# Kernel tuning notes

Measured on AMD Instinct MI355X. Metric: run time of the kernel, lower is better.

Reference implementation:

```python
import jax, jax.numpy as jnp
import numpy as np

N, D = 1024, 1024          # sensors, raw signal length
EMB, CC, TP, NH, L, FF = 128, 64, 16, 4, 2, 2048
HD = EMB // NH             # head dim = 32


def setup_inputs() -> dict:
    key = jax.random.key(0)
    ks = iter(jax.random.split(key, 64))
    rn = lambda shape, s=0.05: jax.random.normal(next(ks), shape, dtype=jnp.float32) * s
    return {
        "x": jax.random.normal(next(ks), (N, 1, D), dtype=jnp.float32),
        "conv1_w": rn((CC // 2, 1, 7), 0.3), "conv1_b": rn((CC // 2,)),
        "bn1_g": jnp.ones((CC // 2,)), "bn1_b": jnp.zeros((CC // 2,)),
        "bn1_m": jnp.zeros((CC // 2,)), "bn1_v": jnp.ones((CC // 2,)),
        "conv2_w": rn((CC, CC // 2, 5), 0.1), "conv2_b": rn((CC,)),
        "bn2_g": jnp.ones((CC,)), "bn2_b": jnp.zeros((CC,)),
        "bn2_m": jnp.zeros((CC,)), "bn2_v": jnp.ones((CC,)),
        "proj_w": rn((EMB, CC * TP)), "proj_b": rn((EMB,)),
        "attn_in_w": rn((L, 3 * EMB, EMB)), "attn_in_b": rn((L, 3 * EMB)),
        "attn_out_w": rn((L, EMB, EMB)), "attn_out_b": rn((L, EMB)),
        "ln1_g": jnp.ones((L, EMB)), "ln1_b": jnp.zeros((L, EMB)),
        "ff1_w": rn((L, FF, EMB)), "ff1_b": rn((L, FF)),
        "ff2_w": rn((L, EMB, FF)), "ff2_b": rn((L, EMB)),
        "ln2_g": jnp.ones((L, EMB)), "ln2_b": jnp.zeros((L, EMB)),
        "nh1_w": rn((EMB, EMB)), "nh1_b": rn((EMB,)),
        "nh2_w": rn((3, EMB)), "nh2_b": rn((3,)),
        "e1_w": rn((EMB, 2 * EMB)), "e1_b": rn((EMB,)),
        "e2_w": rn((1, EMB)), "e2_b": rn((1,)),
        "p1_w": rn((EMB, EMB)), "p1_b": rn((EMB,)),
        "p2_w": rn((EMB, EMB)), "p2_b": rn((EMB,)),
    }


def _conv1d(x, w, b, pad):
    y = jax.lax.conv_general_dilated(x, w, (1,), [(pad, pad)],
                                     dimension_numbers=("NCH", "OIH", "NCH"))
    return y + b[None, :, None]


def _bn(x, g, b, m, v):  # eval-mode BatchNorm1d, eps=1e-5
    return (x - m[None, :, None]) * (g / jnp.sqrt(v + 1e-5))[None, :, None] + b[None, :, None]


def _ln(x, g, b):  # LayerNorm over last dim, eps=1e-5
    mu = x.mean(-1, keepdims=True)
    var = ((x - mu) ** 2).mean(-1, keepdims=True)
    return (x - mu) / jnp.sqrt(var + 1e-5) * g + b


def reference(x, conv1_w, conv1_b, bn1_g, bn1_b, bn1_m, bn1_v,
              conv2_w, conv2_b, bn2_g, bn2_b, bn2_m, bn2_v,
              proj_w, proj_b, attn_in_w, attn_in_b, attn_out_w, attn_out_b,
              ln1_g, ln1_b, ff1_w, ff1_b, ff2_w, ff2_b, ln2_g, ln2_b,
              nh1_w, nh1_b, nh2_w, nh2_b, e1_w, e1_b, e2_w, e2_b,
              p1_w, p1_b, p2_w, p2_b):
    # ---- SensorTemporalEncoder: conv+BN+GELU x2, AdaptiveAvgPool1d(TP) ----
    h = jax.nn.gelu(_bn(_conv1d(x, conv1_w, conv1_b, 3), bn1_g, bn1_b, bn1_m, bn1_v), approximate=False)
    h = jax.nn.gelu(_bn(_conv1d(h, conv2_w, conv2_b, 2), bn2_g, bn2_b, bn2_m, bn2_v), approximate=False)
    h = h.reshape(N, CC, TP, D // TP).mean(-1)  # adaptive avg pool (D divisible by TP)
    z = h.reshape(N, CC * TP) @ proj_w.T + proj_b  # (N, EMB)

    # ---- TransformerEncoder (post-LN, relu FFN, eval: no dropout) ----
    t = z
    for l in range(L):
        qkv = t @ attn_in_w[l].T + attn_in_b[l]          # (N, 3*EMB)
        q, k, v = jnp.split(qkv, 3, axis=-1)
        q = q.reshape(N, NH, HD).transpose(1, 0, 2)      # (H, N, d)
        k = k.reshape(N, NH, HD).transpose(1, 0, 2)
        v = v.reshape(N, NH, HD).transpose(1, 0, 2)
        a = jax.nn.softmax(jnp.einsum("hnd,hmd->hnm", q, k) / (HD ** 0.5), axis=-1)
        o = jnp.einsum("hnm,hmd->hnd", a, v).transpose(1, 0, 2).reshape(N, EMB)
        t = _ln(t + o @ attn_out_w[l].T + attn_out_b[l], ln1_g[l], ln1_b[l])
        f = jax.nn.relu(t @ ff1_w[l].T + ff1_b[l]) @ ff2_w[l].T + ff2_b[l]
        t = _ln(t + f, ln2_g[l], ln2_b[l])

    # ---- node head ----
    node_logits = jax.nn.relu(t @ nh1_w.T + nh1_b) @ nh2_w.T + nh2_b  # (N, 3)

    # ---- all-pairs edge MLP: cat([hi,hj]) @ W1 == hi@W1[:,:E] + hj@W1[:,E:] ----
    hi = t @ e1_w[:, :EMB].T                 # (N, EMB)
    hj = t @ e1_w[:, EMB:].T                 # (N, EMB)
    pre = hi[:, None, :] + hj[None, :, :] + e1_b  # (N, N, EMB)
    edge_logits = (jax.nn.relu(pre) @ e2_w[0]) + e2_b[0]  # (N, N)

    # ---- projector on pre-transformer z ----
    proj = jax.nn.relu(z @ p1_w.T + p1_b) @ p2_w.T + p2_b  # (N, EMB)
    return (node_logits, edge_logits, proj)
```

## Files before the change

kernel.cpp:

```cpp
#include <hip/hip_runtime.h>
#include <math.h>


typedef float f32x4 __attribute__((ext_vector_type(4)));
typedef short bf16x8 __attribute__((ext_vector_type(8)));
typedef unsigned short u16;
typedef unsigned short us4 __attribute__((ext_vector_type(4)));

__device__ __forceinline__ float gelu_fast(float v) {
  float ax = fabsf(v) * 0.70710678118654752440f;
  float t = __builtin_amdgcn_rcpf(fmaf(0.3275911f, ax, 1.f));
  float p = fmaf(1.061405429f, t, -1.453152027f);
  p = fmaf(p, t, 1.421413741f);
  p = fmaf(p, t, -0.284496736f);
  p = fmaf(p, t, 0.254829592f);
  p = p * t;
  float e = __expf(-ax * ax);
  float erfa = fmaf(-p, e, 1.f);
  float erfv = copysignf(erfa, v);
  return 0.5f * v * (1.f + erfv);
}

__device__ __forceinline__ u16 to_bf16(float v) {
  unsigned int u = __float_as_uint(v);
  return (u16)((u + 0x7FFFu + ((u >> 16) & 1u)) >> 16);
}

__global__ __launch_bounds__(256) void encoder_kernel(
    const float* __restrict__ x,
    const float* __restrict__ w1, const float* __restrict__ b1,
    const float* __restrict__ g1, const float* __restrict__ be1,
    const float* __restrict__ m1, const float* __restrict__ v1,
    const float* __restrict__ w2, const float* __restrict__ b2,
    const float* __restrict__ g2, const float* __restrict__ be2,
    const float* __restrict__ m2, const float* __restrict__ v2,
    u16* __restrict__ pooled_bf)
{
  const int blk = blockIdx.x;
  const int n = blk >> 1, hb = blk & 1;
  const int P0 = hb * 512;
  const int tid = threadIdx.x;

  __shared__ __align__(16) float xs[524];
  __shared__ __align__(16) u16 h1s[516 * 40];

  for (int s = tid; s < 522; s += 256) {
    int gp = P0 - 5 + s;
    xs[s] = (gp >= 0 && gp < 1024) ? x[n * 1024 + gp] : 0.f;
  }

  const int l = tid & 63;
  const int w = tid >> 6;
  const int col = l & 15;
  const int kh = l >> 4;
  const int oc = w * 16 + col;
  bf16x8 bf[5];
#pragma unroll
  for (int t = 0; t < 5; t++) {
#pragma unroll
    for (int e = 0; e < 8; e++)
      bf[t][e] = (short)to_bf16(w2[(oc * 32 + kh * 8 + e) * 5 + t]);
  }
  const float sc2 = g2[oc] * rsqrtf(v2[oc] + 1e-5f);
  const float sh2 = (b2[oc] - m2[oc]) * sc2 + be2[oc];

  const int ch = tid & 31;
  float wk[7];
#pragma unroll
  for (int k = 0; k < 7; k++) wk[k] = w1[ch * 7 + k];
  const float s1 = g1[ch] * rsqrtf(v1[ch] + 1e-5f);
  const float t1 = (b1[ch] - m1[ch]) * s1 + be1[ch];

  __syncthreads();

  const int rb = tid >> 5;
  for (int r = rb; r < 516; r += 8) {
    float acc = 0.f;
#pragma unroll
    for (int k = 0; k < 7; k++) acc += wk[k] * xs[r + k];
    int pos = P0 - 2 + r;
    u16 hv = to_bf16(gelu_fast(fmaf(acc, s1, t1)));
    h1s[r * 40 + ch] = (pos >= 0 && pos < 1024) ? hv : (u16)0;
  }
  __syncthreads();

  float pool = 0.f;
#pragma unroll 4
  for (int pt = 0; pt < 32; pt++) {
    f32x4 acc = {0.f, 0.f, 0.f, 0.f};
    const u16* ap = &h1s[(pt * 16 + col) * 40 + kh * 8];
#pragma unroll
    for (int t = 0; t < 5; t++) {
      bf16x8 af = *(const bf16x8*)(ap + t * 40);
      acc = __builtin_amdgcn_mfma_f32_16x16x32_bf16(af, bf[t], acc, 0, 0, 0);
    }
    float s = 0.f;
#pragma unroll
    for (int rr = 0; rr < 4; rr++) s += gelu_fast(fmaf(acc[rr], sc2, sh2));
    pool += s;
    if ((pt & 3) == 3) {
      pool += __shfl_xor(pool, 16);
      pool += __shfl_xor(pool, 32);
      if (l < 16)
        pooled_bf[(n * 64 + oc) * 16 + hb * 8 + (pt >> 2)] =
            to_bf16(pool * (1.f / 64.f));
      pool = 0.f;
    }
  }
}

template<int NR, bool BF32, bool RELU, bool VT>
__global__ __launch_bounds__(64) void mm_kernel(
    const u16* __restrict__ A, int lda, long long zA,
    const void* __restrict__ Bv, int ldb, long long zB,
    const float* __restrict__ bias,
    const float* __restrict__ Res,
    float* __restrict__ Cf, u16* __restrict__ Cb, u16* __restrict__ vt,
    int ldc, long long zC, int K, float scale)
{
  const int z = blockIdx.z;
  const int m0 = blockIdx.x * 32, n0 = blockIdx.y * (NR * 16);
  const int l = threadIdx.x;
  const int r = l & 15, kh = l >> 4;

  A += (size_t)z * zA;
  f32x4 acc[2][NR];
#pragma unroll
  for (int i = 0; i < 2; i++)
#pragma unroll
    for (int j = 0; j < NR; j++) acc[i][j] = (f32x4){0.f, 0.f, 0.f, 0.f};

  const u16* Ap0 = A + (size_t)(m0 + r) * lda + kh * 8;
  const u16* Ap1 = Ap0 + (size_t)16 * lda;
  const float* Bf = (const float*)Bv + (BF32 ? (size_t)z * zB + (size_t)(n0 + r) * ldb + kh * 8 : 0);
  const u16*  Bb = (const u16*)Bv  + (BF32 ? 0 : (size_t)z * zB + (size_t)(n0 + r) * ldb + kh * 8);

  for (int k0 = 0; k0 < K; k0 += 32) {
    bf16x8 a0 = *(const bf16x8*)(Ap0 + k0);
    bf16x8 a1 = *(const bf16x8*)(Ap1 + k0);
    bf16x8 bfr[NR];
#pragma unroll
    for (int ni = 0; ni < NR; ni++) {
      if (BF32) {
        const float* bp = Bf + (size_t)ni * 16 * ldb + k0;
        float4 w0 = *(const float4*)bp;
        float4 w1 = *(const float4*)(bp + 4);
        bfr[ni][0] = (short)to_bf16(w0.x); bfr[ni][1] = (short)to_bf16(w0.y);
        bfr[ni][2] = (short)to_bf16(w0.z); bfr[ni][3] = (short)to_bf16(w0.w);
        bfr[ni][4] = (short)to_bf16(w1.x); bfr[ni][5] = (short)to_bf16(w1.y);
        bfr[ni][6] = (short)to_bf16(w1.z); bfr[ni][7] = (short)to_bf16(w1.w);
      } else {
        bfr[ni] = *(const bf16x8*)(Bb + (size_t)ni * 16 * ldb + k0);
      }
    }
#pragma unroll
    for (int ni = 0; ni < NR; ni++) {
      acc[0][ni] = __builtin_amdgcn_mfma_f32_16x16x32_bf16(a0, bfr[ni], acc[0][ni], 0, 0, 0);
      acc[1][ni] = __builtin_amdgcn_mfma_f32_16x16x32_bf16(a1, bfr[ni], acc[1][ni], 0, 0, 0);
    }
  }

  if (Cf) Cf += (size_t)z * zC;
  if (Cb) Cb += (size_t)z * zC;
#pragma unroll
  for (int mi = 0; mi < 2; mi++) {
#pragma unroll
    for (int ni = 0; ni < NR; ni++) {
#pragma unroll
      for (int reg = 0; reg < 4; reg++) {
        int row = m0 + mi * 16 + kh * 4 + reg;
        int colx = n0 + ni * 16 + r;
        float v = acc[mi][ni][reg] * scale;
        if (bias) v += bias[colx];
        if (Res) v += Res[(size_t)row * ldc + colx];
        if (RELU) v = fmaxf(v, 0.f);
        if (Cf) Cf[(size_t)row * ldc + colx] = v;
        if (Cb) Cb[(size_t)row * ldc + colx] = to_bf16(v);
        if (VT) {
          if (colx >= 256) {
            int hv = (colx - 256) >> 5, dv = (colx - 256) & 31;
            vt[(size_t)hv * 32768 + (size_t)dv * 1024 + row] = to_bf16(v);
          }
        }
      }
    }
  }
}

__global__ __launch_bounds__(256) void softmax_kernel(float* __restrict__ S)
{
  int row = blockIdx.x * 4 + (threadIdx.x >> 6);
  int lane = threadIdx.x & 63;
  float* p = S + (size_t)row * 1024 + lane * 4;
  float4 v[4];
  float mx = -3.4e38f;
#pragma unroll
  for (int j = 0; j < 4; j++) {
    v[j] = *(float4*)(p + j * 256);
    mx = fmaxf(mx, fmaxf(fmaxf(v[j].x, v[j].y), fmaxf(v[j].z, v[j].w)));
  }
#pragma unroll
  for (int off = 32; off >= 1; off >>= 1) mx = fmaxf(mx, __shfl_xor(mx, off));
  float sum = 0.f;
#pragma unroll
  for (int j = 0; j < 4; j++) {
    v[j].x = __expf(v[j].x - mx); v[j].y = __expf(v[j].y - mx);
    v[j].z = __expf(v[j].z - mx); v[j].w = __expf(v[j].w - mx);
    sum += v[j].x + v[j].y + v[j].z + v[j].w;
  }
#pragma unroll
  for (int off = 32; off >= 1; off >>= 1) sum += __shfl_xor(sum, off);
  float inv = 1.f / sum;
  u16* q = (u16*)S + (size_t)row * 2048;
#pragma unroll
  for (int j = 0; j < 4; j++) {
    us4 o;
    o[0] = to_bf16(v[j].x * inv); o[1] = to_bf16(v[j].y * inv);
    o[2] = to_bf16(v[j].z * inv); o[3] = to_bf16(v[j].w * inv);
    *(us4*)(q + lane * 4 + j * 256) = o;
  }
}

__global__ __launch_bounds__(256) void ln_kernel(
    const float* __restrict__ in, float* __restrict__ out, u16* __restrict__ outb,
    const float* __restrict__ g, const float* __restrict__ b)
{
  int row = blockIdx.x * 4 + (threadIdx.x >> 6);
  int lane = threadIdx.x & 63;
  const float* p = in + (size_t)row * 128 + lane * 2;
  float2 v = *(const float2*)p;
  float s = v.x + v.y;
#pragma unroll
  for (int off = 32; off >= 1; off >>= 1) s += __shfl_xor(s, off);
  float mu = s * (1.f / 128.f);
  float dx = v.x - mu, dy = v.y - mu;
  float q = dx * dx + dy * dy;
#pragma unroll
  for (int off = 32; off >= 1; off >>= 1) q += __shfl_xor(q, off);
  float inv = rsqrtf(q * (1.f / 128.f) + 1e-5f);
  float2 gv = *(const float2*)(g + lane * 2);
  float2 bv = *(const float2*)(b + lane * 2);
  float ox = dx * inv * gv.x + bv.x, oy = dy * inv * gv.y + bv.y;
  size_t idx = (size_t)row * 128 + lane * 2;
  out[idx] = ox; out[idx + 1] = oy;
  outb[idx] = to_bf16(ox); outb[idx + 1] = to_bf16(oy);
}

__global__ __launch_bounds__(256) void nh2_kernel(
    const float* __restrict__ mid, const float* __restrict__ w,
    const float* __restrict__ b, float* __restrict__ out)
{
  int m = blockIdx.x * 256 + threadIdx.x;
  const float* row = mid + (size_t)m * 128;
  float a0 = 0.f, a1 = 0.f, a2 = 0.f;
#pragma unroll 4
  for (int k = 0; k < 128; k++) {
    float xv = row[k];
    a0 += xv * w[k]; a1 += xv * w[128 + k]; a2 += xv * w[256 + k];
  }
  out[m * 3 + 0] = a0 + b[0];
  out[m * 3 + 1] = a1 + b[1];
  out[m * 3 + 2] = a2 + b[2];
}

__global__ __launch_bounds__(256) void edge_kernel(
    const float* __restrict__ hi, const float* __restrict__ hjb,
    const float* __restrict__ w, const float* __restrict__ e2b,
    float* __restrict__ out)
{
  const int i0 = blockIdx.x * 64;
  const int j0 = blockIdx.y * 32;
  __shared__ float his[128][64];
  __shared__ float hjs[128][32];
  const int tid = threadIdx.x;
  {
    int r = tid >> 2, c0 = (tid & 3) * 32;
#pragma unroll
    for (int u = 0; u < 8; u++) {
      float4 v = *(const float4*)(hi + (size_t)(i0 + r) * 128 + c0 + u * 4);
      his[c0 + u * 4 + 0][r] = v.x; his[c0 + u * 4 + 1][r] = v.y;
      his[c0 + u * 4 + 2][r] = v.z; his[c0 + u * 4 + 3][r] = v.w;
    }
  }
  {
    int r = tid >> 3, c0 = (tid & 7) * 16;
#pragma unroll
    for (int u = 0; u < 4; u++) {
      float4 v = *(const float4*)(hjb + (size_t)(j0 + r) * 128 + c0 + u * 4);
      hjs[c0 + u * 4 + 0][r] = v.x; hjs[c0 + u * 4 + 1][r] = v.y;
      hjs[c0 + u * 4 + 2][r] = v.z; hjs[c0 + u * 4 + 3][r] = v.w;
    }
  }
  __syncthreads();
  const int il = (tid & 15) * 4, jl = (tid >> 4) * 2;
  float acc[4][2] = {{0.f,0.f},{0.f,0.f},{0.f,0.f},{0.f,0.f}};
  for (int e = 0; e < 128; e++) {
    float4 a = *(const float4*)&his[e][il];
    float2 bv = *(const float2*)&hjs[e][jl];
    float we = w[e];
    float av[4] = {a.x, a.y, a.z, a.w};
    float bb[2] = {bv.x, bv.y};
#pragma unroll
    for (int ii = 0; ii < 4; ii++)
#pragma unroll
      for (int jj = 0; jj < 2; jj++)
        acc[ii][jj] += fmaxf(av[ii] + bb[jj], 0.f) * we;
  }
  float eb = e2b[0];
#pragma unroll
  for (int ii = 0; ii < 4; ii++) {
    float2 vv = make_float2(acc[ii][0] + eb, acc[ii][1] + eb);
    *(float2*)(out + (size_t)(i0 + il + ii) * 1024 + j0 + jl) = vv;
  }
}

extern "C" void kernel_launch(void* const* d_in, const int* in_sizes, int n_in,
                              void* d_out, int out_size, void* d_ws, size_t ws_size,
                              hipStream_t stream)
{
  const float* x        = (const float*)d_in[0];
  const float* conv1_w  = (const float*)d_in[1];
  const float* conv1_b  = (const float*)d_in[2];
  const float* bn1_g    = (const float*)d_in[3];
  const float* bn1_b    = (const float*)d_in[4];
  const float* bn1_m    = (const float*)d_in[5];
  const float* bn1_v    = (const float*)d_in[6];
  const float* conv2_w  = (const float*)d_in[7];
  const float* conv2_b  = (const float*)d_in[8];
  const float* bn2_g    = (const float*)d_in[9];
  const float* bn2_b    = (const float*)d_in[10];
  const float* bn2_m    = (const float*)d_in[11];
  const float* bn2_v    = (const float*)d_in[12];
  const float* proj_w   = (const float*)d_in[13];
  const float* proj_b   = (const float*)d_in[14];
  const float* attn_in_w  = (const float*)d_in[15];
  const float* attn_in_b  = (const float*)d_in[16];
  const float* attn_out_w = (const float*)d_in[17];
  const float* attn_out_b = (const float*)d_in[18];
  const float* ln1_g    = (const float*)d_in[19];
  const float* ln1_b    = (const float*)d_in[20];
  const float* ff1_w    = (const float*)d_in[21];
  const float* ff1_b    = (const float*)d_in[22];
  const float* ff2_w    = (const float*)d_in[23];
  const float* ff2_b    = (const float*)d_in[24];
  const float* ln2_g    = (const float*)d_in[25];
  const float* ln2_b    = (const float*)d_in[26];
  const float* nh1_w    = (const float*)d_in[27];
  const float* nh1_b    = (const float*)d_in[28];
  const float* nh2_w    = (const float*)d_in[29];
  const float* nh2_b    = (const float*)d_in[30];
  const float* e1_w     = (const float*)d_in[31];
  const float* e1_b     = (const float*)d_in[32];
  const float* e2_w     = (const float*)d_in[33];
  const float* e2_b     = (const float*)d_in[34];
  const float* p1_w     = (const float*)d_in[35];
  const float* p1_b     = (const float*)d_in[36];
  const float* p2_w     = (const float*)d_in[37];
  const float* p2_b     = (const float*)d_in[38];

  float* ws = (float*)d_ws;

  const bool full = (ws_size >= (size_t)20 * 1024 * 1024);
  const size_t RN = full ? 4194304 : 1048576;
  float* R     = ws;
  float* z     = ws + RN;
  u16*  z_bf   = (u16*)(z + 131072);
  float* tS    = z + 131072 + 65536;
  u16*  t_bf   = (u16*)(tS + 131072);
  float* pre   = tS + 131072 + 65536;
  u16*  qkv_bf = (u16*)(pre + 131072);
  u16*  vt     = qkv_bf + 393216;
  u16*  attnO  = vt + 131072;
  u16*  pooled_bf = (u16*)R;
  float* Sb    = R;
  u16*  fb     = (u16*)R;
  float* hib   = R;
  float* hjbb  = R + 131072;
  float* nhmid = R + 262144;
  u16*  pmid   = (u16*)(R + 393216);

  float* out_node = (float*)d_out;
  float* out_edge = out_node + 3072;
  float* out_proj = out_edge + 1048576;

  const float iso = 0.17677669529663689f;
  float* nullf = nullptr; u16* nullb = nullptr;

  encoder_kernel<<<2048, 256, 0, stream>>>(
      x, conv1_w, conv1_b, bn1_g, bn1_b, bn1_m, bn1_v,
      conv2_w, conv2_b, bn2_g, bn2_b, bn2_m, bn2_v, pooled_bf);

  mm_kernel<2, true, false, false><<<dim3(32, 4), 64, 0, stream>>>(
      pooled_bf, 1024, 0, proj_w, 1024, 0, proj_b, nullf,
      z, z_bf, nullb, 128, 0, 1024, 1.f);

  for (int l = 0; l < 2; l++) {
    const float* tin = l ? tS : z;
    const u16* tin_bf = l ? t_bf : z_bf;
    mm_kernel<4, true, false, true><<<dim3(32, 6), 64, 0, stream>>>(
        tin_bf, 128, 0, attn_in_w + l * 49152, 128, 0, attn_in_b + l * 384,
        nullf, nullf, qkv_bf, vt, 384, 0, 128, 1.f);

    if (full) {
      mm_kernel<4, false, false, false><<<dim3(32, 16, 4), 64, 0, stream>>>(
          qkv_bf, 384, 32, qkv_bf + 128, 384, 32, nullf, nullf,
          Sb, nullb, nullb, 1024, 1048576LL, 32, iso);
      softmax_kernel<<<1024, 256, 0, stream>>>(Sb);
      mm_kernel<2, false, false, false><<<dim3(32, 1, 4), 64, 0, stream>>>(
          (const u16*)Sb, 2048, 2097152LL, vt, 1024, 32768LL, nullf, nullf,
          nullf, attnO, nullb, 128, 32LL, 1024, 1.f);
    } else {
      for (int h = 0; h < 4; h++) {
        mm_kernel<4, false, false, false><<<dim3(32, 16, 1), 64, 0, stream>>>(
            qkv_bf + h * 32, 384, 0, qkv_bf + 128 + h * 32, 384, 0,
            nullf, nullf, Sb, nullb, nullb, 1024, 0, 32, iso);
        softmax_kernel<<<256, 256, 0, stream>>>(Sb);
        mm_kernel<2, false, false, false><<<dim3(32, 1, 1), 64, 0, stream>>>(
            (const u16*)Sb, 2048, 0, vt + h * 32768, 1024, 0, nullf, nullf,
            nullf, attnO + h * 32, nullb, 128, 0, 1024, 1.f);
      }
    }

    mm_kernel<2, true, false, false><<<dim3(32, 4), 64, 0, stream>>>(
        attnO, 128, 0, attn_out_w + l * 16384, 128, 0, attn_out_b + l * 128,
        tin, pre, nullb, nullb, 128, 0, 128, 1.f);
    ln_kernel<<<256, 256, 0, stream>>>(pre, tS, t_bf, ln1_g + l * 128, ln1_b + l * 128);

    mm_kernel<4, true, true, false><<<dim3(32, 32), 64, 0, stream>>>(
        t_bf, 128, 0, ff1_w + l * 262144, 128, 0, ff1_b + l * 2048,
        nullf, nullf, fb, nullb, 2048, 0, 128, 1.f);
    mm_kernel<2, true, false, false><<<dim3(32, 4), 64, 0, stream>>>(
        fb, 2048, 0, ff2_w + l * 262144, 2048, 0, ff2_b + l * 128,
        tS, pre, nullb, nullb, 128, 0, 2048, 1.f);
    ln_kernel<<<256, 256, 0, stream>>>(pre, tS, t_bf, ln2_g + l * 128, ln2_b + l * 128);
  }

  mm_kernel<2, true, true, false><<<dim3(32, 4), 64, 0, stream>>>(
      t_bf, 128, 0, nh1_w, 128, 0, nh1_b, nullf,
      nhmid, nullb, nullb, 128, 0, 128, 1.f);
  nh2_kernel<<<4, 256, 0, stream>>>(nhmid, nh2_w, nh2_b, out_node);

  mm_kernel<2, true, false, false><<<dim3(32, 4), 64, 0, stream>>>(
      t_bf, 128, 0, e1_w, 256, 0, nullf, nullf,
      hib, nullb, nullb, 128, 0, 128, 1.f);
  mm_kernel<2, true, false, false><<<dim3(32, 4), 64, 0, stream>>>(
      t_bf, 128, 0, e1_w + 128, 256, 0, e1_b, nullf,
      hjbb, nullb, nullb, 128, 0, 128, 1.f);
  edge_kernel<<<dim3(16, 32), 256, 0, stream>>>(hib, hjbb, e2_w, e2_b, out_edge);

  mm_kernel<2, true, true, false><<<dim3(32, 4), 64, 0, stream>>>(
      z_bf, 128, 0, p1_w, 128, 0, p1_b, nullf,
      nullf, pmid, nullb, 128, 0, 128, 1.f);
  mm_kernel<2, true, false, false><<<dim3(32, 4), 64, 0, stream>>>(
      pmid, 128, 0, p2_w, 128, 0, p2_b, nullf,
      out_proj, nullb, nullb, 128, 0, 128, 1.f);
}
```

Measured before the change: 492.3 us.

## Fuse attention into flash kernel, fuse out-proj/FF2 with LayerNorm, pre-convert weights to bf16

Replaces the separate QK^T GEMM, softmax and PV GEMM with a single online-softmax attention kernel that never materialises the 1024x1024 score matrix. The attention-output and FF2 GEMMs now take residual-add and LayerNorm into a shared-memory epilogue, removing the standalone LN kernels. All weights are converted to bf16 once per call by a new kernel instead of inside every GEMM's inner loop, and the two edge projections are merged into one GEMM. This trades extra launch work for the weight conversion and lower parallelism in the fused kernels (32 blocks for the LN-fused GEMMs, 256 for attention) for far less memory traffic.

```diff
diff --git a/kernel.cpp b/kernel.cpp
--- a/kernel.cpp
+++ b/kernel.cpp
@@ -6,6 +6,7 @@
 typedef short bf16x8 __attribute__((ext_vector_type(8)));
 typedef unsigned short u16;
 typedef unsigned short us4 __attribute__((ext_vector_type(4)));
+typedef unsigned int u32;
 
 __device__ __forceinline__ float gelu_fast(float v) {
   float ax = fabsf(v) * 0.70710678118654752440f;
@@ -22,8 +23,11 @@
 }
 
 __device__ __forceinline__ u16 to_bf16(float v) {
-  unsigned int u = __float_as_uint(v);
+  u32 u = __float_as_uint(v);
   return (u16)((u + 0x7FFFu + ((u >> 16) & 1u)) >> 16);
+}
+__device__ __forceinline__ u32 packbf(float a, float b) {
+  return (u32)to_bf16(a) | ((u32)to_bf16(b) << 16);
 }
 
 __global__ __launch_bounds__(256) void encoder_kernel(
@@ -109,21 +113,79 @@
   }
 }
 
-template<int NR, bool BF32, bool RELU, bool VT>
+__global__ __launch_bounds__(256) void wconv_kernel(
+    const float* __restrict__ proj_w, const float* __restrict__ attn_in_w,
+    const float* __restrict__ attn_out_w, const float* __restrict__ ff1_w,
+    const float* __restrict__ ff2_w, const float* __restrict__ nh1_w,
+    const float* __restrict__ e1_w, const float* __restrict__ e1_b,
+    const float* __restrict__ p1_w, const float* __restrict__ p2_w,
+    u16* __restrict__ wbf, float* __restrict__ wbias)
+{
+  if (blockIdx.x == 1360) {
+    int j = threadIdx.x;
+    wbias[j] = (j < 128) ? 0.f : e1_b[j - 128];
+    return;
+  }
+  int i0 = (blockIdx.x * 256 + threadIdx.x) * 4;
+  float v[4];
+  if (i0 < 131072) {
+    const float* s = proj_w + i0;
+#pragma unroll
+    for (int u = 0; u < 4; u++) v[u] = s[u];
+  } else if (i0 < 229376) {
+    const float* s = attn_in_w + (i0 - 131072);
+#pragma unroll
+    for (int u = 0; u < 4; u++) v[u] = s[u];
+  } else if (i0 < 262144) {
+    const float* s = attn_out_w + (i0 - 229376);
+#pragma unroll
+    for (int u = 0; u < 4; u++) v[u] = s[u];
+  } else if (i0 < 786432) {
+    const float* s = ff1_w + (i0 - 262144);
+#pragma unroll
+    for (int u = 0; u < 4; u++) v[u] = s[u];
+  } else if (i0 < 1310720) {
+    const float* s = ff2_w + (i0 - 786432);
+#pragma unroll
+    for (int u = 0; u < 4; u++) v[u] = s[u];
+  } else if (i0 < 1327104) {
+    const float* s = nh1_w + (i0 - 1310720);
+#pragma unroll
+    for (int u = 0; u < 4; u++) v[u] = s[u];
+  } else if (i0 < 1359872) {
+    int j = i0 - 1327104;
+#pragma unroll
+    for (int u = 0; u < 4; u++) {
+      int idx = j + u, nn = idx >> 7, k = idx & 127;
+      v[u] = e1_w[(nn & 127) * 256 + (nn >> 7) * 128 + k];
+    }
+  } else if (i0 < 1376256) {
+    const float* s = p1_w + (i0 - 1359872);
+#pragma unroll
+    for (int u = 0; u < 4; u++) v[u] = s[u];
+  } else {
+    const float* s = p2_w + (i0 - 1376256);
+#pragma unroll
+    for (int u = 0; u < 4; u++) v[u] = s[u];
+  }
+  us4 o;
+#pragma unroll
+  for (int u = 0; u < 4; u++) o[u] = to_bf16(v[u]);
+  *(us4*)(wbf + i0) = o;
+}
+
+template<int NR, bool RELU, bool VT>
 __global__ __launch_bounds__(64) void mm_kernel(
-    const u16* __restrict__ A, int lda, long long zA,
-    const void* __restrict__ Bv, int ldb, long long zB,
+    const u16* __restrict__ A, int lda,
+    const u16* __restrict__ B, int ldb,
     const float* __restrict__ bias,
-    const float* __restrict__ Res,
     float* __restrict__ Cf, u16* __restrict__ Cb, u16* __restrict__ vt,
-    int ldc, long long zC, int K, float scale)
-{
-  const int z = blockIdx.z;
+    int ldc, int K)
+{
   const int m0 = blockIdx.x * 32, n0 = blockIdx.y * (NR * 16);
   const int l = threadIdx.x;
   const int r = l & 15, kh = l >> 4;
 
-  A += (size_t)z * zA;
   f32x4 acc[2][NR];
 #pragma unroll
   for (int i = 0; i < 2; i++)
@@ -132,27 +194,15 @@
 
   const u16* Ap0 = A + (size_t)(m0 + r) * lda + kh * 8;
   const u16* Ap1 = Ap0 + (size_t)16 * lda;
-  const float* Bf = (const float*)Bv + (BF32 ? (size_t)z * zB + (size_t)(n0 + r) * ldb + kh * 8 : 0);
-  const u16*  Bb = (const u16*)Bv  + (BF32 ? 0 : (size_t)z * zB + (size_t)(n0 + r) * ldb + kh * 8);
+  const u16* Bp = B + (size_t)(n0 + r) * ldb + kh * 8;
 
   for (int k0 = 0; k0 < K; k0 += 32) {
     bf16x8 a0 = *(const bf16x8*)(Ap0 + k0);
     bf16x8 a1 = *(const bf16x8*)(Ap1 + k0);
     bf16x8 bfr[NR];
 #pragma unroll
-    for (int ni = 0; ni < NR; ni++) {
-      if (BF32) {
-        const float* bp = Bf + (size_t)ni * 16 * ldb + k0;
-        float4 w0 = *(const float4*)bp;
-        float4 w1 = *(const float4*)(bp + 4);
-        bfr[ni][0] = (short)to_bf16(w0.x); bfr[ni][1] = (short)to_bf16(w0.y);
-        bfr[ni][2] = (short)to_bf16(w0.z); bfr[ni][3] = (short)to_bf16(w0.w);
-        bfr[ni][4] = (short)to_bf16(w1.x); bfr[ni][5] = (short)to_bf16(w1.y);
-        bfr[ni][6] = (short)to_bf16(w1.z); bfr[ni][7] = (short)to_bf16(w1.w);
-      } else {
-        bfr[ni] = *(const bf16x8*)(Bb + (size_t)ni * 16 * ldb + k0);
-      }
-    }
+    for (int ni = 0; ni < NR; ni++)
+      bfr[ni] = *(const bf16x8*)(Bp + (size_t)ni * 16 * ldb + k0);
 #pragma unroll
     for (int ni = 0; ni < NR; ni++) {
       acc[0][ni] = __builtin_amdgcn_mfma_f32_16x16x32_bf16(a0, bfr[ni], acc[0][ni], 0, 0, 0);
@@ -160,8 +210,6 @@
     }
   }
 
-  if (Cf) Cf += (size_t)z * zC;
-  if (Cb) Cb += (size_t)z * zC;
 #pragma unroll
   for (int mi = 0; mi < 2; mi++) {
 #pragma unroll
@@ -170,9 +218,8 @@
       for (int reg = 0; reg < 4; reg++) {
         int row = m0 + mi * 16 + kh * 4 + reg;
         int colx = n0 + ni * 16 + r;
-        float v = acc[mi][ni][reg] * scale;
+        float v = acc[mi][ni][reg];
         if (bias) v += bias[colx];
-        if (Res) v += Res[(size_t)row * ldc + colx];
         if (RELU) v = fmaxf(v, 0.f);
         if (Cf) Cf[(size_t)row * ldc + colx] = v;
         if (Cb) Cb[(size_t)row * ldc + colx] = to_bf16(v);
@@ -187,63 +234,157 @@
   }
 }
 
-__global__ __launch_bounds__(256) void softmax_kernel(float* __restrict__ S)
-{
-  int row = blockIdx.x * 4 + (threadIdx.x >> 6);
-  int lane = threadIdx.x & 63;
-  float* p = S + (size_t)row * 1024 + lane * 4;
-  float4 v[4];
-  float mx = -3.4e38f;
-#pragma unroll
-  for (int j = 0; j < 4; j++) {
-    v[j] = *(float4*)(p + j * 256);
-    mx = fmaxf(mx, fmaxf(fmaxf(v[j].x, v[j].y), fmaxf(v[j].z, v[j].w)));
-  }
-#pragma unroll
-  for (int off = 32; off >= 1; off >>= 1) mx = fmaxf(mx, __shfl_xor(mx, off));
-  float sum = 0.f;
-#pragma unroll
-  for (int j = 0; j < 4; j++) {
-    v[j].x = __expf(v[j].x - mx); v[j].y = __expf(v[j].y - mx);
-    v[j].z = __expf(v[j].z - mx); v[j].w = __expf(v[j].w - mx);
-    sum += v[j].x + v[j].y + v[j].z + v[j].w;
-  }
-#pragma unroll
-  for (int off = 32; off >= 1; off >>= 1) sum += __shfl_xor(sum, off);
-  float inv = 1.f / sum;
-  u16* q = (u16*)S + (size_t)row * 2048;
-#pragma unroll
-  for (int j = 0; j < 4; j++) {
-    us4 o;
-    o[0] = to_bf16(v[j].x * inv); o[1] = to_bf16(v[j].y * inv);
-    o[2] = to_bf16(v[j].z * inv); o[3] = to_bf16(v[j].w * inv);
-    *(us4*)(q + lane * 4 + j * 256) = o;
-  }
-}
-
-__global__ __launch_bounds__(256) void ln_kernel(
-    const float* __restrict__ in, float* __restrict__ out, u16* __restrict__ outb,
-    const float* __restrict__ g, const float* __restrict__ b)
-{
-  int row = blockIdx.x * 4 + (threadIdx.x >> 6);
-  int lane = threadIdx.x & 63;
-  const float* p = in + (size_t)row * 128 + lane * 2;
-  float2 v = *(const float2*)p;
-  float s = v.x + v.y;
-#pragma unroll
-  for (int off = 32; off >= 1; off >>= 1) s += __shfl_xor(s, off);
-  float mu = s * (1.f / 128.f);
-  float dx = v.x - mu, dy = v.y - mu;
-  float q = dx * dx + dy * dy;
-#pragma unroll
-  for (int off = 32; off >= 1; off >>= 1) q += __shfl_xor(q, off);
-  float inv = rsqrtf(q * (1.f / 128.f) + 1e-5f);
-  float2 gv = *(const float2*)(g + lane * 2);
-  float2 bv = *(const float2*)(b + lane * 2);
-  float ox = dx * inv * gv.x + bv.x, oy = dy * inv * gv.y + bv.y;
-  size_t idx = (size_t)row * 128 + lane * 2;
-  out[idx] = ox; out[idx + 1] = oy;
-  outb[idx] = to_bf16(ox); outb[idx + 1] = to_bf16(oy);
+__global__ __launch_bounds__(64) void attn_kernel(
+    const u16* __restrict__ qkv, const u16* __restrict__ vt,
+    u16* __restrict__ attnO)
+{
+  const int h = blockIdx.y, q0 = blockIdx.x * 16;
+  const int l = threadIdx.x, q = l & 15, g = l >> 4;
+  const float iso = 0.17677669529663689f;
+
+  bf16x8 qf = *(const bf16x8*)(qkv + (size_t)(q0 + q) * 384 + h * 32 + g * 8);
+  const int kvo0 = 8 * (q >> 2) + (q & 3);
+  const int kvo1 = kvo0 + 4;
+  const u16* kbase = qkv + 128 + h * 32 + g * 8;
+  const u16* vbase = vt + (size_t)h * 32768 + (size_t)q * 1024 + g * 8;
+
+  f32x4 o0 = {0.f, 0.f, 0.f, 0.f}, o1 = {0.f, 0.f, 0.f, 0.f};
+  float m = -1e30f, lsum = 0.f;
+  const f32x4 zero = {0.f, 0.f, 0.f, 0.f};
+
+  for (int kv0 = 0; kv0 < 1024; kv0 += 32) {
+    bf16x8 k0f = *(const bf16x8*)(kbase + (size_t)(kv0 + kvo0) * 384);
+    bf16x8 k1f = *(const bf16x8*)(kbase + (size_t)(kv0 + kvo1) * 384);
+    f32x4 s0 = __builtin_amdgcn_mfma_f32_16x16x32_bf16(k0f, qf, zero, 0, 0, 0);
+    f32x4 s1 = __builtin_amdgcn_mfma_f32_16x16x32_bf16(k1f, qf, zero, 0, 0, 0);
+
+    float tm = fmaxf(fmaxf(fmaxf(s0[0], s0[1]), fmaxf(s0[2], s0[3])),
+                     fmaxf(fmaxf(s1[0], s1[1]), fmaxf(s1[2], s1[3])));
+    tm = fmaxf(tm, __shfl_xor(tm, 16));
+    tm = fmaxf(tm, __shfl_xor(tm, 32));
+    float mn = fmaxf(m, tm);
+    float corr = __expf((m - mn) * iso);
+
+    float e0[4], e1v[4], sum = 0.f;
+#pragma unroll
+    for (int j = 0; j < 4; j++) {
+      e0[j] = __expf((s0[j] - mn) * iso);
+      e1v[j] = __expf((s1[j] - mn) * iso);
+      sum += e0[j] + e1v[j];
+    }
+    lsum = lsum * corr + sum;
+#pragma unroll
+    for (int j = 0; j < 4; j++) { o0[j] *= corr; o1[j] *= corr; }
+
+    union { u32 u[4]; bf16x8 v; } P;
+    P.u[0] = packbf(e0[0], e0[1]);
+    P.u[1] = packbf(e0[2], e0[3]);
+    P.u[2] = packbf(e1v[0], e1v[1]);
+    P.u[3] = packbf(e1v[2], e1v[3]);
+
+    bf16x8 v0 = *(const bf16x8*)(vbase + kv0);
+    bf16x8 v1 = *(const bf16x8*)(vbase + 16 * 1024 + kv0);
+    o0 = __builtin_amdgcn_mfma_f32_16x16x32_bf16(v0, P.v, o0, 0, 0, 0);
+    o1 = __builtin_amdgcn_mfma_f32_16x16x32_bf16(v1, P.v, o1, 0, 0, 0);
+    m = mn;
+  }
+  lsum += __shfl_xor(lsum, 16);
+  lsum += __shfl_xor(lsum, 32);
+  float inv = __builtin_amdgcn_rcpf(lsum);
+
+  us4 w0, w1;
+#pragma unroll
+  for (int reg = 0; reg < 4; reg++) {
+    w0[reg] = to_bf16(o0[reg] * inv);
+    w1[reg] = to_bf16(o1[reg] * inv);
+  }
+  u16* outp = attnO + (size_t)(q0 + q) * 128 + h * 32 + 4 * g;
+  *(us4*)outp = w0;
+  *(us4*)(outp + 16) = w1;
+}
+
+template<int K>
+__global__ __launch_bounds__(256) void owl_kernel(
+    const u16* __restrict__ A, const u16* __restrict__ Bw,
+    const float* __restrict__ bias, const float* __restrict__ Res,
+    float* __restrict__ outF, u16* __restrict__ outB,
+    const float* __restrict__ g_, const float* __restrict__ b_)
+{
+  __shared__ float ld[32][132];
+  const int m0 = blockIdx.x * 32;
+  const int tid = threadIdx.x;
+  const int w = tid >> 6, l = tid & 63;
+  const int r = l & 15, kg = l >> 4;
+
+  f32x4 acc[2][2];
+#pragma unroll
+  for (int i = 0; i < 2; i++)
+#pragma unroll
+    for (int j = 0; j < 2; j++) acc[i][j] = (f32x4){0.f, 0.f, 0.f, 0.f};
+
+  const u16* Ap0 = A + (size_t)(m0 + r) * K + kg * 8;
+  const u16* Ap1 = Ap0 + (size_t)16 * K;
+  const u16* Bp0 = Bw + (size_t)(w * 32 + r) * K + kg * 8;
+  const u16* Bp1 = Bp0 + (size_t)16 * K;
+
+#pragma unroll 4
+  for (int k0 = 0; k0 < K; k0 += 32) {
+    bf16x8 a0 = *(const bf16x8*)(Ap0 + k0);
+    bf16x8 a1 = *(const bf16x8*)(Ap1 + k0);
+    bf16x8 b0 = *(const bf16x8*)(Bp0 + k0);
+    bf16x8 b1 = *(const bf16x8*)(Bp1 + k0);
+    acc[0][0] = __builtin_amdgcn_mfma_f32_16x16x32_bf16(a0, b0, acc[0][0], 0, 0, 0);
+    acc[0][1] = __builtin_amdgcn_mfma_f32_16x16x32_bf16(a0, b1, acc[0][1], 0, 0, 0);
+    acc[1][0] = __builtin_amdgcn_mfma_f32_16x16x32_bf16(a1, b0, acc[1][0], 0, 0, 0);
+    acc[1][1] = __builtin_amdgcn_mfma_f32_16x16x32_bf16(a1, b1, acc[1][1], 0, 0, 0);
+  }
+
+#pragma unroll
+  for (int mi = 0; mi < 2; mi++)
+#pragma unroll
+    for (int ni = 0; ni < 2; ni++)
+#pragma unroll
+      for (int reg = 0; reg < 4; reg++) {
+        int row = mi * 16 + kg * 4 + reg;
+        int col = w * 32 + ni * 16 + r;
+        ld[row][col] = acc[mi][ni][reg] + bias[col] +
+                       Res[(size_t)(m0 + row) * 128 + col];
+      }
+  __syncthreads();
+
+  const int row = tid >> 3, s8 = tid & 7;
+  f32x4 vv[4];
+  float sum = 0.f, ss = 0.f;
+#pragma unroll
+  for (int u = 0; u < 4; u++) {
+    vv[u] = *(const f32x4*)&ld[row][s8 * 16 + u * 4];
+#pragma unroll
+    for (int j = 0; j < 4; j++) { sum += vv[u][j]; ss += vv[u][j] * vv[u][j]; }
+  }
+#pragma unroll
+  for (int off = 1; off <= 4; off <<= 1) {
+    sum += __shfl_xor(sum, off);
+    ss += __shfl_xor(ss, off);
+  }
+  float mu = sum * (1.f / 128.f);
+  float var = ss * (1.f / 128.f) - mu * mu;
+  float inv = rsqrtf(var + 1e-5f);
+  size_t base = (size_t)(m0 + row) * 128;
+#pragma unroll
+  for (int u = 0; u < 4; u++) {
+    int c = s8 * 16 + u * 4;
+    f32x4 gv = *(const f32x4*)(g_ + c);
+    f32x4 bv = *(const f32x4*)(b_ + c);
+    f32x4 o;
+    us4 ob;
+#pragma unroll
+    for (int j = 0; j < 4; j++) {
+      o[j] = (vv[u][j] - mu) * inv * gv[j] + bv[j];
+      ob[j] = to_bf16(o[j]);
+    }
+    *(f32x4*)(outF + base + c) = o;
+    *(us4*)(outB + base + c) = ob;
+  }
 }
 
 __global__ __launch_bounds__(256) void nh2_kernel(
@@ -264,7 +405,7 @@
 }
 
 __global__ __launch_bounds__(256) void edge_kernel(
-    const float* __restrict__ hi, const float* __restrict__ hjb,
+    const float* __restrict__ comb,
     const float* __restrict__ w, const float* __restrict__ e2b,
     float* __restrict__ out)
 {
@@ -277,7 +418,7 @@
     int r = tid >> 2, c0 = (tid & 3) * 32;
 #pragma unroll
     for (int u = 0; u < 8; u++) {
-      float4 v = *(const float4*)(hi + (size_t)(i0 + r) * 128 + c0 + u * 4);
+      float4 v = *(const float4*)(comb + (size_t)(i0 + r) * 256 + c0 + u * 4);
       his[c0 + u * 4 + 0][r] = v.x; his[c0 + u * 4 + 1][r] = v.y;
       his[c0 + u * 4 + 2][r] = v.z; his[c0 + u * 4 + 3][r] = v.w;
     }
@@ -286,7 +427,7 @@
     int r = tid >> 3, c0 = (tid & 7) * 16;
 #pragma unroll
     for (int u = 0; u < 4; u++) {
-      float4 v = *(const float4*)(hjb + (size_t)(j0 + r) * 128 + c0 + u * 4);
+      float4 v = *(const float4*)(comb + (size_t)(j0 + r) * 256 + 128 + c0 + u * 4);
       hjs[c0 + u * 4 + 0][r] = v.x; hjs[c0 + u * 4 + 1][r] = v.y;
       hjs[c0 + u * 4 + 2][r] = v.z; hjs[c0 + u * 4 + 3][r] = v.w;
     }
@@ -360,98 +501,67 @@
 
   float* ws = (float*)d_ws;
 
-  const bool full = (ws_size >= (size_t)20 * 1024 * 1024);
-  const size_t RN = full ? 4194304 : 1048576;
-  float* R     = ws;
-  float* z     = ws + RN;
-  u16*  z_bf   = (u16*)(z + 131072);
-  float* tS    = z + 131072 + 65536;
-  u16*  t_bf   = (u16*)(tS + 131072);
-  float* pre   = tS + 131072 + 65536;
-  u16*  qkv_bf = (u16*)(pre + 131072);
-  u16*  vt     = qkv_bf + 393216;
-  u16*  attnO  = vt + 131072;
+  u16*  wbf    = (u16*)ws;
+  float* wbias = ws + 696320;
+  float* z     = ws + 696576;
+  u16*  z_bf   = (u16*)(ws + 827648);
+  float* tS    = ws + 893184;
+  u16*  t_bf   = (u16*)(ws + 1024256);
+  u16*  qkv_bf = (u16*)(ws + 1089792);
+  float* R     = ws + 1286400;
   u16*  pooled_bf = (u16*)R;
-  float* Sb    = R;
+  u16*  attnO  = (u16*)R;
+  u16*  vt     = (u16*)R + 131072;
   u16*  fb     = (u16*)R;
-  float* hib   = R;
-  float* hjbb  = R + 131072;
-  float* nhmid = R + 262144;
+  float* nhmid = R;
+  float* e1out = R + 131072;
   u16*  pmid   = (u16*)(R + 393216);
 
   float* out_node = (float*)d_out;
   float* out_edge = out_node + 3072;
   float* out_proj = out_edge + 1048576;
 
-  const float iso = 0.17677669529663689f;
   float* nullf = nullptr; u16* nullb = nullptr;
+
+  wconv_kernel<<<1361, 256, 0, stream>>>(
+      proj_w, attn_in_w, attn_out_w, ff1_w, ff2_w, nh1_w, e1_w, e1_b,
+      p1_w, p2_w, wbf, wbias);
 
   encoder_kernel<<<2048, 256, 0, stream>>>(
       x, conv1_w, conv1_b, bn1_g, bn1_b, bn1_m, bn1_v,
       conv2_w, conv2_b, bn2_g, bn2_b, bn2_m, bn2_v, pooled_bf);
 
-  mm_kernel<2, true, false, false><<<dim3(32, 4), 64, 0, stream>>>(
-      pooled_bf, 1024, 0, proj_w, 1024, 0, proj_b, nullf,
-      z, z_bf, nullb, 128, 0, 1024, 1.f);
+  mm_kernel<2, false, false><<<dim3(32, 4), 64, 0, stream>>>(
+      pooled_bf, 1024, wbf, 1024, proj_b, z, z_bf, nullb, 128, 1024);
 
   for (int l = 0; l < 2; l++) {
-    const float* tin = l ? tS : z;
+    const float* resIn = l ? tS : z;
     const u16* tin_bf = l ? t_bf : z_bf;
-    mm_kernel<4, true, false, true><<<dim3(32, 6), 64, 0, stream>>>(
-        tin_bf, 128, 0, attn_in_w + l * 49152, 128, 0, attn_in_b + l * 384,
-        nullf, nullf, qkv_bf, vt, 384, 0, 128, 1.f);
-
-    if (full) {
-      mm_kernel<4, false, false, false><<<dim3(32, 16, 4), 64, 0, stream>>>(
-          qkv_bf, 384, 32, qkv_bf + 128, 384, 32, nullf, nullf,
-          Sb, nullb, nullb, 1024, 1048576LL, 32, iso);
-      softmax_kernel<<<1024, 256, 0, stream>>>(Sb);
-      mm_kernel<2, false, false, false><<<dim3(32, 1, 4), 64, 0, stream>>>(
-          (const u16*)Sb, 2048, 2097152LL, vt, 1024, 32768LL, nullf, nullf,
-          nullf, attnO, nullb, 128, 32LL, 1024, 1.f);
-    } else {
-      for (int h = 0; h < 4; h++) {
-        mm_kernel<4, false, false, false><<<dim3(32, 16, 1), 64, 0, stream>>>(
-            qkv_bf + h * 32, 384, 0, qkv_bf + 128 + h * 32, 384, 0,
-            nullf, nullf, Sb, nullb, nullb, 1024, 0, 32, iso);
-        softmax_kernel<<<256, 256, 0, stream>>>(Sb);
-        mm_kernel<2, false, false, false><<<dim3(32, 1, 1), 64, 0, stream>>>(
-            (const u16*)Sb, 2048, 0, vt + h * 32768, 1024, 0, nullf, nullf,
-            nullf, attnO + h * 32, nullb, 128, 0, 1024, 1.f);
-      }
-    }
-
-    mm_kernel<2, true, false, false><<<dim3(32, 4), 64, 0, stream>>>(
-        attnO, 128, 0, attn_out_w + l * 16384, 128, 0, attn_out_b + l * 128,
-        tin, pre, nullb, nullb, 128, 0, 128, 1.f);
-    ln_kernel<<<256, 256, 0, stream>>>(pre, tS, t_bf, ln1_g + l * 128, ln1_b + l * 128);
-
-    mm_kernel<4, true, true, false><<<dim3(32, 32), 64, 0, stream>>>(
-        t_bf, 128, 0, ff1_w + l * 262144, 128, 0, ff1_b + l * 2048,
-        nullf, nullf, fb, nullb, 2048, 0, 128, 1.f);
-    mm_kernel<2, true, false, false><<<dim3(32, 4), 64, 0, stream>>>(
-        fb, 2048, 0, ff2_w + l * 262144, 2048, 0, ff2_b + l * 128,
-        tS, pre, nullb, nullb, 128, 0, 2048, 1.f);
-    ln_kernel<<<256, 256, 0, stream>>>(pre, tS, t_bf, ln2_g + l * 128, ln2_b + l * 128);
-  }
-
-  mm_kernel<2, true, true, false><<<dim3(32, 4), 64, 0, stream>>>(
-      t_bf, 128, 0, nh1_w, 128, 0, nh1_b, nullf,
-      nhmid, nullb, nullb, 128, 0, 128, 1.f);
+    mm_kernel<4, false, true><<<dim3(32, 6), 64, 0, stream>>>(
+        tin_bf, 128, wbf + 131072 + l * 49152, 128, attn_in_b + l * 384,
+        nullf, qkv_bf, vt, 384, 128);
+    attn_kernel<<<dim3(64, 4), 64, 0, stream>>>(qkv_bf, vt, attnO);
+    owl_kernel<128><<<32, 256, 0, stream>>>(
+        attnO, wbf + 229376 + l * 16384, attn_out_b + l * 128, resIn,
+        tS, t_bf, ln1_g + l * 128, ln1_b + l * 128);
+    mm_kernel<4, true, false><<<dim3(32, 32), 64, 0, stream>>>(
+        t_bf, 128, wbf + 262144 + l * 262144, 128, ff1_b + l * 2048,
+        nullf, fb, nullb, 2048, 128);
+    owl_kernel<2048><<<32, 256, 0, stream>>>(
+        fb, wbf + 786432 + l * 262144, ff2_b + l * 128, tS,
+        tS, t_bf, ln2_g + l * 128, ln2_b + l * 128);
+  }
+
+  mm_kernel<2, true, false><<<dim3(32, 4), 64, 0, stream>>>(
+      t_bf, 128, wbf + 1310720, 128, nh1_b, nhmid, nullb, nullb, 128, 128);
   nh2_kernel<<<4, 256, 0, stream>>>(nhmid, nh2_w, nh2_b, out_node);
 
-  mm_kernel<2, true, false, false><<<dim3(32, 4), 64, 0, stream>>>(
-      t_bf, 128, 0, e1_w, 256, 0, nullf, nullf,
-      hib, nullb, nullb, 128, 0, 128, 1.f);
-  mm_kernel<2, true, false, false><<<dim3(32, 4), 64, 0, stream>>>(
-      t_bf, 128, 0, e1_w + 128, 256, 0, e1_b, nullf,
-      hjbb, nullb, nullb, 128, 0, 128, 1.f);
-  edge_kernel<<<dim3(16, 32), 256, 0, stream>>>(hib, hjbb, e2_w, e2_b, out_edge);
-
-  mm_kernel<2, true, true, false><<<dim3(32, 4), 64, 0, stream>>>(
-      z_bf, 128, 0, p1_w, 128, 0, p1_b, nullf,
-      nullf, pmid, nullb, 128, 0, 128, 1.f);
-  mm_kernel<2, true, false, false><<<dim3(32, 4), 64, 0, stream>>>(
-      pmid, 128, 0, p2_w, 128, 0, p2_b, nullf,
-      out_proj, nullb, nullb, 128, 0, 128, 1.f);
-}
+  mm_kernel<2, false, false><<<dim3(32, 8), 64, 0, stream>>>(
+      t_bf, 128, wbf + 1327104, 128, wbias, e1out, nullb, nullb, 256, 128);
+  edge_kernel<<<dim3(16, 32), 256, 0, stream>>>(e1out, e2_w, e2_b, out_edge);
+
+  mm_kernel<2, true, false><<<dim3(32, 4), 64, 0, stream>>>(
+      z_bf, 128, wbf + 1359872, 128, p1_b, nullf, pmid, nullb, 128, 128);
+  mm_kernel<2, false, false><<<dim3(32, 4), 64, 0, stream>>>(
+      pmid, 128, wbf + 1376256, 128, p2_b, out_proj, nullb, nullb, 128, 128);
+}
```

Measured after the change: 447.6 us. -9.1%, faster.
